# Optimization experiments

Measured on AMD Instinct MI355X. Metric: run time of the kernel, lower is better.

## Reference

```python
import jax, jax.numpy as jnp
import numpy as np


def setup_inputs() -> dict:
    key = jax.random.key(0)
    k1, k2, k3, k4 = jax.random.split(key, 4)
    B, T, H = 32, 2048, 1024
    decoder_output = jax.random.normal(k1, (B, H), dtype=jnp.float32)
    encoder_outputs = jax.random.normal(k2, (B, T, H), dtype=jnp.float32)
    # nn.Linear(H, H): weight [H_out, H_in], bias [H_out]
    W = jax.random.normal(k3, (H, H), dtype=jnp.float32) * (1.0 / np.sqrt(H))
    b = jax.random.normal(k4, (H,), dtype=jnp.float32) * 0.01
    return {"decoder_output": decoder_output, "encoder_outputs": encoder_outputs, "W": W, "b": b}


def reference(decoder_output, encoder_outputs, W, b):
    # 'general' attention: energy[b,t] = dec[b] . (Linear(enc[b,t]))
    # Linear(x) = x @ W.T + b
    projected = jnp.einsum('bth,oh->bto', encoder_outputs, W) + b  # [B,T,H]
    energies = jnp.einsum('bth,bh->bt', projected, decoder_output)  # [B,T]
    attn = jax.nn.softmax(energies, axis=1)
    return attn[..., None]  # [B,T,1]
```

## Files before the change

kernel.cpp:

```cpp
#include <hip/hip_runtime.h>
#include <math.h>

#define BB 32
#define TT 2048
#define HH 1024

__global__ __launch_bounds__(256)
void proj_vec_kernel(const float* __restrict__ dec,
                     const float* __restrict__ W,
                     float* __restrict__ v) {
    const int tid  = threadIdx.x;
    const int lane = tid & 63;
    const int wave = tid >> 6;
    const int h0   = blockIdx.x * 64;
    const int b0   = blockIdx.y * 2;

    __shared__ float sdec[2][HH];
    {
        const float4* src = reinterpret_cast<const float4*>(dec + (size_t)b0 * HH);
        float4* dst = reinterpret_cast<float4*>(&sdec[0][0]);
        dst[tid]       = src[tid];
        dst[tid + 256] = src[tid + 256];
    }
    __syncthreads();

    const int o0 = wave * 256;
    const float* sd0 = &sdec[0][o0];
    const float* sd1 = &sdec[1][o0];
    const float* Wcol = W + (size_t)o0 * HH + h0 + lane;

    float a0 = 0.f, a1 = 0.f;
#pragma unroll 4
    for (int oo = 0; oo < 256; oo += 4) {
        float4 d0 = *reinterpret_cast<const float4*>(sd0 + oo);
        float4 d1 = *reinterpret_cast<const float4*>(sd1 + oo);
        float w0 = Wcol[(size_t)(oo + 0) * HH];
        float w1 = Wcol[(size_t)(oo + 1) * HH];
        float w2 = Wcol[(size_t)(oo + 2) * HH];
        float w3 = Wcol[(size_t)(oo + 3) * HH];
        a0 += d0.x * w0 + d0.y * w1 + d0.z * w2 + d0.w * w3;
        a1 += d1.x * w0 + d1.y * w1 + d1.z * w2 + d1.w * w3;
    }

    __shared__ float red[4][2][64];
    red[wave][0][lane] = a0;
    red[wave][1][lane] = a1;
    __syncthreads();
    if (tid < 128) {
        const int b = tid >> 6;
        v[(size_t)(b0 + b) * HH + h0 + lane] =
            (red[0][b][lane] + red[1][b][lane]) +
            (red[2][b][lane] + red[3][b][lane]);
    }
}

__global__ __launch_bounds__(256)
void energy_kernel(const float* __restrict__ enc,
                   const float* __restrict__ v,
                   float* __restrict__ energy) {
    const int wave = threadIdx.x >> 6;
    const int lane = threadIdx.x & 63;
    const int b    = blockIdx.y;
    const int wid  = blockIdx.x * 4 + wave;
    const int t0   = wid * 8;

    const float4* v4 = reinterpret_cast<const float4*>(v + b * HH);
    const float4 w0 = v4[0 * 64 + lane];
    const float4 w1 = v4[1 * 64 + lane];
    const float4 w2 = v4[2 * 64 + lane];
    const float4 w3 = v4[3 * 64 + lane];

    const float4* ebase =
        reinterpret_cast<const float4*>(enc + ((size_t)b * TT + t0) * HH);

#pragma unroll 2
    for (int r = 0; r < 8; ++r) {
        const float4* e4 = ebase + (size_t)r * (HH / 4);
        float4 e0 = e4[0 * 64 + lane];
        float4 e1 = e4[1 * 64 + lane];
        float4 e2 = e4[2 * 64 + lane];
        float4 e3 = e4[3 * 64 + lane];
        float acc = e0.x * w0.x + e0.y * w0.y + e0.z * w0.z + e0.w * w0.w;
        acc += e1.x * w1.x + e1.y * w1.y + e1.z * w1.z + e1.w * w1.w;
        acc += e2.x * w2.x + e2.y * w2.y + e2.z * w2.z + e2.w * w2.w;
        acc += e3.x * w3.x + e3.y * w3.y + e3.z * w3.z + e3.w * w3.w;
#pragma unroll
        for (int off = 32; off > 0; off >>= 1) acc += __shfl_down(acc, off, 64);
        if (lane == 0) energy[b * TT + t0 + r] = acc;
    }
}

__global__ __launch_bounds__(256)
void softmax_kernel(const float* __restrict__ energy,
                    float* __restrict__ out) {
    const int b   = blockIdx.x;
    const int tid = threadIdx.x;
    const float* e = energy + b * TT;
    float vals[8];
    float m = -INFINITY;
#pragma unroll
    for (int k = 0; k < 8; ++k) {
        vals[k] = e[tid + k * 256];
        m = fmaxf(m, vals[k]);
    }
    __shared__ float redm[4];
    __shared__ float reds[4];
#pragma unroll
    for (int off = 32; off > 0; off >>= 1) m = fmaxf(m, __shfl_xor(m, off, 64));
    if ((tid & 63) == 0) redm[tid >> 6] = m;
    __syncthreads();
    m = fmaxf(fmaxf(redm[0], redm[1]), fmaxf(redm[2], redm[3]));

    float s = 0.f;
#pragma unroll
    for (int k = 0; k < 8; ++k) {
        vals[k] = __expf(vals[k] - m);
        s += vals[k];
    }
#pragma unroll
    for (int off = 32; off > 0; off >>= 1) s += __shfl_xor(s, off, 64);
    if ((tid & 63) == 0) reds[tid >> 6] = s;
    __syncthreads();
    s = reds[0] + reds[1] + reds[2] + reds[3];
    const float inv = 1.0f / s;
#pragma unroll
    for (int k = 0; k < 8; ++k) out[b * TT + tid + k * 256] = vals[k] * inv;
}

extern "C" void kernel_launch(void* const* d_in, const int* in_sizes, int n_in,
                              void* d_out, int out_size, void* d_ws, size_t ws_size,
                              hipStream_t stream) {
    const float* dec = (const float*)d_in[0];
    const float* enc = (const float*)d_in[1];
    const float* W   = (const float*)d_in[2];
    float* out = (float*)d_out;

    float* v      = (float*)d_ws;
    float* energy = v + BB * HH;

    proj_vec_kernel<<<dim3(HH / 64, BB / 2), 256, 0, stream>>>(dec, W, v);
    energy_kernel<<<dim3(64, BB), 256, 0, stream>>>(enc, v, energy);
    softmax_kernel<<<BB, 256, 0, stream>>>(energy, out);
}
```

Baseline: 58.73 us.

## Fuse softmax into energy kernel via last-block atomic counter; nontemporal loads

Merges the softmax into the energy kernel. Each batch row has a counter that proj_vec resets, and the last of its 64 blocks to finish, detected with an atomic, runs the softmax for that row. This removes one kernel launch and the gap between launches. It also switches the streaming encoder loads to nontemporal loads and batches the 8 row reductions so the shuffles interleave. The cost is fences, atomics and some tail serialization, since one block per row does the softmax at the end.

```diff
diff --git a/kernel.cpp b/kernel.cpp
--- a/kernel.cpp
+++ b/kernel.cpp
@@ -5,15 +5,20 @@
 #define TT 2048
 #define HH 1024
 
+typedef float f32x4 __attribute__((ext_vector_type(4)));
+
 __global__ __launch_bounds__(256)
 void proj_vec_kernel(const float* __restrict__ dec,
                      const float* __restrict__ W,
-                     float* __restrict__ v) {
+                     float* __restrict__ v,
+                     int* __restrict__ cnt) {
     const int tid  = threadIdx.x;
     const int lane = tid & 63;
     const int wave = tid >> 6;
     const int h0   = blockIdx.x * 64;
     const int b0   = blockIdx.y * 2;
+
+    if (blockIdx.x == 0 && blockIdx.y == 0 && tid < BB) cnt[tid] = 0;
 
     __shared__ float sdec[2][HH];
     {
@@ -55,9 +60,11 @@
 }
 
 __global__ __launch_bounds__(256)
-void energy_kernel(const float* __restrict__ enc,
-                   const float* __restrict__ v,
-                   float* __restrict__ energy) {
+void energy_softmax_kernel(const float* __restrict__ enc,
+                           const float* __restrict__ v,
+                           float* __restrict__ energy,
+                           int* __restrict__ cnt,
+                           float* __restrict__ out) {
     const int wave = threadIdx.x >> 6;
     const int lane = threadIdx.x & 63;
     const int b    = blockIdx.y;
@@ -70,37 +77,56 @@
     const float4 w2 = v4[2 * 64 + lane];
     const float4 w3 = v4[3 * 64 + lane];
 
-    const float4* ebase =
-        reinterpret_cast<const float4*>(enc + ((size_t)b * TT + t0) * HH);
+    const f32x4* ebase =
+        reinterpret_cast<const f32x4*>(enc + ((size_t)b * TT + t0) * HH);
 
-#pragma unroll 2
+    float racc[8];
+#pragma unroll
     for (int r = 0; r < 8; ++r) {
-        const float4* e4 = ebase + (size_t)r * (HH / 4);
-        float4 e0 = e4[0 * 64 + lane];
-        float4 e1 = e4[1 * 64 + lane];
-        float4 e2 = e4[2 * 64 + lane];
-        float4 e3 = e4[3 * 64 + lane];
-        float acc = e0.x * w0.x + e0.y * w0.y + e0.z * w0.z + e0.w * w0.w;
-        acc += e1.x * w1.x + e1.y * w1.y + e1.z * w1.z + e1.w * w1.w;
-        acc += e2.x * w2.x + e2.y * w2.y + e2.z * w2.z + e2.w * w2.w;
-        acc += e3.x * w3.x + e3.y * w3.y + e3.z * w3.z + e3.w * w3.w;
+        const f32x4* e4 = ebase + (size_t)r * (HH / 4);
+        f32x4 e0 = __builtin_nontemporal_load(e4 + 0 * 64 + lane);
+        f32x4 e1 = __builtin_nontemporal_load(e4 + 1 * 64 + lane);
+        f32x4 e2 = __builtin_nontemporal_load(e4 + 2 * 64 + lane);
+        f32x4 e3 = __builtin_nontemporal_load(e4 + 3 * 64 + lane);
+        float p0 = e0.x * w0.x + e0.y * w0.y + e0.z * w0.z + e0.w * w0.w;
+        float p1 = e1.x * w1.x + e1.y * w1.y + e1.z * w1.z + e1.w * w1.w;
+        float p2 = e2.x * w2.x + e2.y * w2.y + e2.z * w2.z + e2.w * w2.w;
+        float p3 = e3.x * w3.x + e3.y * w3.y + e3.z * w3.z + e3.w * w3.w;
+        racc[r] = (p0 + p1) + (p2 + p3);
+    }
+
 #pragma unroll
-        for (int off = 32; off > 0; off >>= 1) acc += __shfl_down(acc, off, 64);
-        if (lane == 0) energy[b * TT + t0 + r] = acc;
+    for (int off = 32; off > 0; off >>= 1) {
+#pragma unroll
+        for (int r = 0; r < 8; ++r) racc[r] += __shfl_xor(racc[r], off, 64);
     }
-}
 
-__global__ __launch_bounds__(256)
-void softmax_kernel(const float* __restrict__ energy,
-                    float* __restrict__ out) {
-    const int b   = blockIdx.x;
+    if (lane < 8) {
+        float myv = racc[0];
+#pragma unroll
+        for (int r = 1; r < 8; ++r) if (lane == r) myv = racc[r];
+        __hip_atomic_store(&energy[b * TT + t0 + lane], myv,
+                           __ATOMIC_RELAXED, __HIP_MEMORY_SCOPE_AGENT);
+    }
+
+    __shared__ int sLast;
+    __syncthreads();
+    if (threadIdx.x == 0) {
+        __threadfence();
+        int prev = atomicAdd(&cnt[b], 1);
+        sLast = (prev == 63) ? 1 : 0;
+    }
+    __syncthreads();
+    if (!sLast) return;
+
+    __threadfence();
     const int tid = threadIdx.x;
-    const float* e = energy + b * TT;
     float vals[8];
     float m = -INFINITY;
 #pragma unroll
     for (int k = 0; k < 8; ++k) {
-        vals[k] = e[tid + k * 256];
+        vals[k] = __hip_atomic_load(&energy[b * TT + tid + k * 256],
+                                    __ATOMIC_RELAXED, __HIP_MEMORY_SCOPE_AGENT);
         m = fmaxf(m, vals[k]);
     }
     __shared__ float redm[4];
@@ -137,8 +163,8 @@
 
     float* v      = (float*)d_ws;
     float* energy = v + BB * HH;
+    int*   cnt    = (int*)(energy + BB * TT);
 
-    proj_vec_kernel<<<dim3(HH / 64, BB / 2), 256, 0, stream>>>(dec, W, v);
-    energy_kernel<<<dim3(64, BB), 256, 0, stream>>>(enc, v, energy);
-    softmax_kernel<<<BB, 256, 0, stream>>>(energy, out);
+    proj_vec_kernel<<<dim3(HH / 64, BB / 2), 256, 0, stream>>>(dec, W, v, cnt);
+    energy_softmax_kernel<<<dim3(64, BB), 256, 0, stream>>>(enc, v, energy, cnt, out);
 }
```

After: 180.8 us. 208% more time.
